# Performance work log

Measured on AMD Instinct MI355X. Metric: run time of the kernel, lower is better.

## Reference

```python
import jax, jax.numpy as jnp
import numpy as np

N, E, G = 50000, 400000, 64   # nodes, edges, graphs
HEADS = 4
F_IN, H1, C3, OUT = 64, 96, 64, 10  # in feats, hidden (3*32), last conv out, classes


def seg_softmax(alpha, index, num_segments):
    # numerically stable softmax over segments (PyG softmax(alpha, edge_index_i))
    amax = jax.ops.segment_max(alpha, index, num_segments)
    amax = jnp.where(jnp.isfinite(amax), amax, 0.0)
    e = jnp.exp(alpha - amax[index])
    denom = jax.ops.segment_sum(e, index, num_segments)
    return e / (denom[index] + 1e-16)


def general_conv(x, src, dst, Wm, bm, att, Ws=None, bs=None):
    # GeneralConv (attention=True, additive, directed_msg, aggr='add')
    C = att.shape[-1]
    m = (x[src] @ Wm + bm).reshape(-1, HEADS, C)              # [E,H,C] gathered messages
    a = jax.nn.leaky_relu((m * att).sum(-1), 0.2)             # [E,H] attention logits
    a = seg_softmax(a, dst, N)                                # segment softmax per dest node
    agg = jax.ops.segment_sum(m * a[..., None], dst, N)       # [N,H,C] scatter-add
    out = agg.mean(axis=1)                                    # head mean -> [N,C]
    if Ws is None:                                            # lin_self = Identity (in==out)
        return out + x
    return out + x @ Ws + bs


def setup_inputs():
    key = jax.random.key(0)
    ks = jax.random.split(key, 16)
    s = 0.05
    return {
        "x": jax.random.normal(ks[0], (N, F_IN), jnp.float32),
        "edge_index": jax.random.randint(ks[1], (2, E), 0, N, jnp.int32),
        "batch": jnp.sort(jax.random.randint(ks[2], (N,), 0, G, jnp.int32)),
        # layer 1: F_IN -> H1
        "Wm1": jax.random.normal(ks[3], (F_IN, HEADS * H1), jnp.float32) * s,
        "bm1": jnp.zeros((HEADS * H1,), jnp.float32),
        "att1": jax.random.normal(ks[4], (HEADS, H1), jnp.float32) * s,
        "Ws1": jax.random.normal(ks[5], (F_IN, H1), jnp.float32) * s,
        "bs1": jnp.zeros((H1,), jnp.float32),
        # layer 2: H1 -> H1 (lin_self = Identity)
        "Wm2": jax.random.normal(ks[6], (H1, HEADS * H1), jnp.float32) * s,
        "bm2": jnp.zeros((HEADS * H1,), jnp.float32),
        "att2": jax.random.normal(ks[7], (HEADS, H1), jnp.float32) * s,
        # layer 3: H1 -> C3
        "Wm3": jax.random.normal(ks[8], (H1, HEADS * C3), jnp.float32) * s,
        "bm3": jnp.zeros((HEADS * C3,), jnp.float32),
        "att3": jax.random.normal(ks[9], (HEADS, C3), jnp.float32) * s,
        "Ws3": jax.random.normal(ks[10], (H1, C3), jnp.float32) * s,
        "bs3": jnp.zeros((C3,), jnp.float32),
        # classifier
        "Wfc": jax.random.normal(ks[11], (C3, OUT), jnp.float32) * s,
        "bfc": jnp.zeros((OUT,), jnp.float32),
    }


def reference(x, edge_index, batch, Wm1, bm1, att1, Ws1, bs1,
              Wm2, bm2, att2, Wm3, bm3, att3, Ws3, bs3, Wfc, bfc):
    src, dst = edge_index[0], edge_index[1]
    h = general_conv(x, src, dst, Wm1, bm1, att1, Ws1, bs1)
    h = general_conv(h, src, dst, Wm2, bm2, att2)
    h = general_conv(h, src, dst, Wm3, bm3, att3, Ws3, bs3)
    # global_mean_pool
    ssum = jax.ops.segment_sum(h, batch, G)
    cnt = jax.ops.segment_sum(jnp.ones((N, 1), h.dtype), batch, G)
    pooled = ssum / jnp.maximum(cnt, 1.0)                      # [G,C3]
    logits = pooled @ Wfc + bfc
    return jax.nn.log_softmax(logits, axis=1)
```

## Files before the change

### kernel.cpp

```cpp
#include <hip/hip_runtime.h>
#include <hip/hip_bf16.h>
#include <stdint.h>

using bf16 = __hip_bfloat16;
typedef __attribute__((ext_vector_type(8))) short bf16x8;
typedef __attribute__((ext_vector_type(4))) float f32x4;
typedef __attribute__((ext_vector_type(2))) float f32x2;

#define NN 50000
#define NE 400000
#define NG 64
#define NHEADS 4
#define FIN 64
#define HID 96
#define CC3 64
#define NOUT 10

#define SCAN_BLOCK 256
#define NPART ((NN + SCAN_BLOCK - 1) / SCAN_BLOCK)
#define GB16 ((NN/16 + 3) / 4)

__device__ __forceinline__ float b2f(bf16 h){ return __bfloat162float(h); }
__device__ __forceinline__ bf16 f2b(float f){ return __float2bfloat16(f); }

#define NTJOBS 5
struct PrepJobs {
  const float* W[NTJOBS]; bf16* WT[NTJOBS]; int K[NTJOBS]; int Nc[NTJOBS];
  const float* LWm[3]; const float* Latt[3]; const float* Lbm[3];
  bf16* LWT[3]; int LK[3]; int LC[3]; int LncMain[3];
  float* lb;
  int* deg; float* psum;
};
__global__ __launch_bounds__(256) void prep_kernel(PrepJobs j){
  int bid = blockIdx.x;
  if (bid < 3){
    int l = bid;
    const float* Wm = j.LWm[l]; const float* att = j.Latt[l]; const float* bm = j.Lbm[l];
    bf16* WT = j.LWT[l];
    int K = j.LK[l], C = j.LC[l], ncMain = j.LncMain[l];
    for (int idx = threadIdx.x; idx < K*4; idx += 256){
      int k = idx >> 2, h = idx & 3;
      float a = 0.f;
      for (int c=0;c<C;++c) a += Wm[(size_t)k*(4*C) + h*C + c] * att[h*C + c];
      WT[(size_t)(ncMain+h)*K + k] = f2b(a);
    }
    for (int idx = threadIdx.x; idx < 12*K; idx += 256){
      int col = ncMain + 4 + idx / K, k = idx % K;
      WT[(size_t)col*K + k] = f2b(0.f);
    }
    if (threadIdx.x < 4){
      int h = threadIdx.x; float a = 0.f;
      for (int c=0;c<C;++c) a += bm[h*C + c] * att[h*C + c];
      j.lb[l*4 + h] = a;
    }
  } else if (bid < 3 + 256){
    int b = bid - 3;
    for (int t=0; t<NTJOBS; ++t){
      int K = j.K[t], Nc = j.Nc[t], total = K*Nc;
      for (int i = b*256 + threadIdx.x; i < total; i += 256*256){
        int k = i / Nc, n = i % Nc;
        j.WT[t][(size_t)n*K + k] = f2b(j.W[t][i]);
      }
    }
  } else if (bid < 3 + 256 + NPART){
    int i = (bid - 3 - 256)*256 + threadIdx.x;
    if (i < NN) j.deg[i] = 0;
  } else {
    for (int i = threadIdx.x; i < NG*CC3; i += 256) j.psum[i] = 0.f;
  }
}

__global__ void deg_kernel(const int* __restrict__ ei, int* __restrict__ deg){
  int e = blockIdx.x*256 + threadIdx.x;
  if (e < NE) atomicAdd(&deg[ei[NE + e]], 1);
}

__global__ __launch_bounds__(256) void scan_part_kernel(const int* __restrict__ deg,
                                                        int* __restrict__ partials){
  int i = blockIdx.x*SCAN_BLOCK + threadIdx.x;
  int v = (i < NN) ? deg[i] : 0;
  __shared__ int ws[4];
  int lane = threadIdx.x & 63, w = threadIdx.x >> 6;
  int s = v;
  #pragma unroll
  for (int m=1;m<64;m<<=1) s += __shfl_xor(s,m);
  if (lane==0) ws[w]=s;
  __syncthreads();
  if (threadIdx.x==0) partials[blockIdx.x] = ws[0]+ws[1]+ws[2]+ws[3];
}

__global__ __launch_bounds__(256) void scan_top_kernel(int* __restrict__ partials,
                                                       int* __restrict__ off){
  __shared__ int buf[256];
  int t = threadIdx.x;
  int v = (t < NPART) ? partials[t] : 0;
  buf[t] = v; __syncthreads();
  for (int s=1;s<256;s<<=1){
    int x = (t>=s) ? buf[t-s] : 0;
    __syncthreads();
    buf[t] += x;
    __syncthreads();
  }
  if (t < NPART) partials[t] = buf[t] - v;
  if (t == 0) off[NN] = buf[255];
}

__global__ __launch_bounds__(256) void scan_final_kernel(const int* __restrict__ deg,
    const int* __restrict__ partials, int* __restrict__ off, int* __restrict__ cursor){
  __shared__ int buf[256];
  int i = blockIdx.x*SCAN_BLOCK + threadIdx.x;
  int t = threadIdx.x;
  int v = (i<NN) ? deg[i] : 0;
  buf[t] = v; __syncthreads();
  for (int s=1;s<256;s<<=1){
    int x = (t>=s) ? buf[t-s] : 0;
    __syncthreads();
    buf[t] += x;
    __syncthreads();
  }
  int ex = partials[blockIdx.x] + buf[t] - v;
  if (i<NN){ off[i]=ex; cursor[i]=ex; }
}

__global__ void scatter_kernel(const int* __restrict__ ei, int* __restrict__ cursor,
                               int* __restrict__ csr_src){
  int e = blockIdx.x*256 + threadIdx.x;
  if (e < NE){
    int d = ei[NE + e];
    int slot = atomicAdd(&cursor[d], 1);
    csr_src[slot] = ei[e];
  }
}

template<int K, bool F32A>
__global__ __launch_bounds__(256) void gemm_mfma(const void* __restrict__ Ap,
    const bf16* __restrict__ WT, const float* __restrict__ biasMain,
    const float* __restrict__ lb4, uint8_t* __restrict__ outMain, int ncMain,
    float* __restrict__ EL, const float* __restrict__ biasSelf,
    bf16* __restrict__ outSelf, int ncSelf, int msgG, int totalU, int UPB)
{
  constexpr int KT = K/32;
  __shared__ unsigned int sbuf[4][16][16];
  const int wave = threadIdx.x >> 6, lane = threadIdx.x & 63;
  const int tile = blockIdx.x*4 + wave;
  if (tile >= NN/16) return;
  const int lm = lane & 15, q = lane >> 4;
  const int nodeRow = tile*16 + lm;
  const int rdRow = lane >> 2, rdCol = lane & 3;
  const int outRow = tile*16 + rdRow;

  bf16x8 xfrag[KT];
  if (F32A){
    const float* Af = (const float*)Ap;
    #pragma unroll
    for (int kt=0; kt<KT; ++kt){
      float4 a0 = *(const float4*)(Af + (size_t)nodeRow*K + kt*32 + q*8);
      float4 a1 = *(const float4*)(Af + (size_t)nodeRow*K + kt*32 + q*8 + 4);
      bf16 tmp[8];
      tmp[0]=f2b(a0.x); tmp[1]=f2b(a0.y); tmp[2]=f2b(a0.z); tmp[3]=f2b(a0.w);
      tmp[4]=f2b(a1.x); tmp[5]=f2b(a1.y); tmp[6]=f2b(a1.z); tmp[7]=f2b(a1.w);
      xfrag[kt] = *(const bf16x8*)tmp;
    }
  } else {
    const bf16* A = (const bf16*)Ap;
    #pragma unroll
    for (int kt=0; kt<KT; ++kt)
      xfrag[kt] = *(const bf16x8*)(A + (size_t)nodeRow*K + kt*32 + q*8);
  }

  const int u0 = blockIdx.y*UPB, u1 = min(u0+UPB, totalU);
  for (int u=u0; u<u1; ++u){
    if (u < msgG){
      #pragma unroll
      for (int t=0;t<4;++t){
        int ct = u*4 + t;
        f32x4 acc = {};
        #pragma unroll
        for (int kt=0; kt<KT; ++kt){
          bf16x8 wfrag = *(const bf16x8*)(WT + (size_t)(ct*16+lm)*K + kt*32 + q*8);
          acc = __builtin_amdgcn_mfma_f32_16x16x32_bf16(wfrag, xfrag[kt], acc, 0,0,0);
        }
        int wc = ct*16 + q*4;
        float v0 = acc[0]+biasMain[wc],   v1 = acc[1]+biasMain[wc+1];
        float v2 = acc[2]+biasMain[wc+2], v3 = acc[3]+biasMain[wc+3];
        int pk = 0;
        pk = __builtin_amdgcn_cvt_pk_fp8_f32(v0, v1, pk, false);
        pk = __builtin_amdgcn_cvt_pk_fp8_f32(v2, v3, pk, true);
        sbuf[wave][lm][t*4 + q] = (unsigned int)pk;
      }
      __builtin_amdgcn_wave_barrier();
      uint4 v = *(uint4*)&sbuf[wave][rdRow][rdCol*4];
      *(uint4*)(outMain + (size_t)outRow*ncMain + u*64 + rdCol*16) = v;
      __builtin_amdgcn_wave_barrier();
    } else if (u == msgG){
      int ct = ncMain/16;
      f32x4 acc = {};
      #pragma unroll
      for (int kt=0; kt<KT; ++kt){
        bf16x8 wfrag = *(const bf16x8*)(WT + (size_t)(ct*16+lm)*K + kt*32 + q*8);
        acc = __builtin_amdgcn_mfma_f32_16x16x32_bf16(wfrag, xfrag[kt], acc, 0,0,0);
      }
      if (q == 0){
        float4 e;
        float l;
        l = acc[0]+lb4[0]; l = (l>=0.f)?l:0.2f*l; e.x = __expf(fminf(fmaxf(l,-60.f),60.f));
        l = acc[1]+lb4[1]; l = (l>=0.f)?l:0.2f*l; e.y = __expf(fminf(fmaxf(l,-60.f),60.f));
        l = acc[2]+lb4[2]; l = (l>=0.f)?l:0.2f*l; e.z = __expf(fminf(fmaxf(l,-60.f),60.f));
        l = acc[3]+lb4[3]; l = (l>=0.f)?l:0.2f*l; e.w = __expf(fminf(fmaxf(l,-60.f),60.f));
        *(float4*)(EL + 4*(size_t)nodeRow) = e;
      }
    } else {
      int sg = u - msgG - 1;
      #pragma unroll
      for (int t=0;t<2;++t){
        int ct = ncMain/16 + 1 + sg*2 + t;
        f32x4 acc = {};
        #pragma unroll
        for (int kt=0; kt<KT; ++kt){
          bf16x8 wfrag = *(const bf16x8*)(WT + (size_t)(ct*16+lm)*K + kt*32 + q*8);
          acc = __builtin_amdgcn_mfma_f32_16x16x32_bf16(wfrag, xfrag[kt], acc, 0,0,0);
        }
        int c = ct*16 + q*4 - ncMain - 16;
        bf16 st[4];
        st[0]=f2b(acc[0]+biasSelf[c]);   st[1]=f2b(acc[1]+biasSelf[c+1]);
        st[2]=f2b(acc[2]+biasSelf[c+2]); st[3]=f2b(acc[3]+biasSelf[c+3]);
        uint2 uu = *(uint2*)st;
        sbuf[wave][lm][t*8 + q*2]     = uu.x;
        sbuf[wave][lm][t*8 + q*2 + 1] = uu.y;
      }
      __builtin_amdgcn_wave_barrier();
      uint4 v = *(uint4*)&sbuf[wave][rdRow][rdCol*4];
      *(uint4*)(outSelf + (size_t)outRow*ncSelf + sg*32 + rdCol*8) = v;
      __builtin_amdgcn_wave_barrier();
    }
  }
}

template<int C>
__global__ __launch_bounds__(256) void conv_agg(const int* __restrict__ off,
    const int* __restrict__ csr_src, const float* __restrict__ EL,
    const uint8_t* __restrict__ M8, const bf16* __restrict__ Hself,
    bf16* __restrict__ Hout)
{
  constexpr int R = 4*C;
  __shared__ float red[4][R];
  const int wave = threadIdx.x >> 6, lane = threadIdx.x & 63;
  const int n = blockIdx.x*4 + wave;
  const int e0 = off[n], e1 = off[n+1];

  const bool active = (8*lane) < R;
  const int hidx = min(3, (8*lane) / C);
  const int myoff = active ? lane*8 : 0;
  float acc[8] = {0,0,0,0,0,0,0,0};
  float dnl = 0.f;

  for (int base=e0; base<e1; base+=8){
    const int cnt8 = min(8, e1-base);
    int sreg = (lane < cnt8) ? csr_src[base+lane] : 0;
    int sv[8];
    #pragma unroll
    for (int j=0;j<8;++j) sv[j] = __shfl(sreg, j);

    float wl[8]; uint2 u[8];
    #pragma unroll
    for (int j=0;j<8;++j){
      wl[j] = EL[4*(size_t)sv[j] + hidx];
      u[j]  = *(const uint2*)(M8 + (size_t)sv[j]*R + myoff);
    }
    #pragma unroll
    for (int j=0;j<8;++j){
      float w = (j < cnt8) ? wl[j] : 0.f;
      dnl += w;
      f32x2 a0 = __builtin_amdgcn_cvt_pk_f32_fp8((int)u[j].x, false);
      f32x2 a1 = __builtin_amdgcn_cvt_pk_f32_fp8((int)u[j].x, true);
      f32x2 a2 = __builtin_amdgcn_cvt_pk_f32_fp8((int)u[j].y, false);
      f32x2 a3 = __builtin_amdgcn_cvt_pk_f32_fp8((int)u[j].y, true);
      acc[0] += a0.x*w;  acc[1] += a0.y*w;
      acc[2] += a1.x*w;  acc[3] += a1.y*w;
      acc[4] += a2.x*w;  acc[5] += a2.y*w;
      acc[6] += a3.x*w;  acc[7] += a3.y*w;
    }
  }

  float rd = 1.f/(dnl + 1e-16f);
  if (active){
    #pragma unroll
    for (int j=0;j<8;++j) red[wave][8*lane+j] = acc[j]*rd;
  }
  __syncthreads();

  for (int c=lane; c<C; c+=64){
    float v = 0.25f*(red[wave][c] + red[wave][C+c] + red[wave][2*C+c] + red[wave][3*C+c]);
    float sv2 = b2f(Hself[(size_t)n*C + c]);
    Hout[(size_t)n*C + c] = f2b(v + sv2);
  }
}

__global__ __launch_bounds__(256) void pool_kernel(const bf16* __restrict__ H3,
    const int* __restrict__ batch, float* __restrict__ psum){
  const int wave = threadIdx.x >> 6, lane = threadIdx.x & 63;
  const int row0 = (blockIdx.x*4 + wave)*64;
  if (row0 >= NN) return;
  const int cnt = min(64, NN - row0);
  int bv = (lane < cnt) ? batch[row0 + lane] : -1;
  int cur = __shfl(bv, 0);
  float acc = 0.f;
  for (int j=0; j<cnt; ++j){
    int g = __shfl(bv, j);
    if (g != cur){ atomicAdd(&psum[cur*CC3 + lane], acc); acc = 0.f; cur = g; }
    acc += b2f(H3[(size_t)(row0 + j)*CC3 + lane]);
  }
  atomicAdd(&psum[cur*CC3 + lane], acc);
}

__global__ __launch_bounds__(64) void fc_kernel(const float* __restrict__ psum,
    const int* __restrict__ batch, const float* __restrict__ Wfc,
    const float* __restrict__ bfc, float* __restrict__ out){
  int g = blockIdx.x, t = threadIdx.x;
  __shared__ int sb[2];
  if (t < 2){
    int target = g + t;
    int lo=0, hi=NN;
    while (lo<hi){ int mid=(lo+hi)>>1; if (batch[mid]<target) lo=mid+1; else hi=mid; }
    sb[t]=lo;
  }
  __syncthreads();
  float cnt = (float)(sb[1]-sb[0]);
  __shared__ float p[CC3];
  __shared__ float lg[NOUT];
  p[t] = psum[g*CC3 + t] / fmaxf(cnt, 1.0f);
  __syncthreads();
  if (t < NOUT){
    float a = bfc[t];
    for (int c=0;c<CC3;++c) a += p[c]*Wfc[c*NOUT + t];
    lg[t] = a;
  }
  __syncthreads();
  if (t < NOUT){
    float m = -INFINITY;
    #pragma unroll
    for (int i=0;i<NOUT;++i) m = fmaxf(m, lg[i]);
    float s = 0.f;
    #pragma unroll
    for (int i=0;i<NOUT;++i) s += __expf(lg[i]-m);
    out[g*NOUT + t] = lg[t] - m - __logf(s);
  }
}

extern "C" void kernel_launch(void* const* d_in, const int* in_sizes, int n_in,
                              void* d_out, int out_size, void* d_ws, size_t ws_size,
                              hipStream_t stream) {
  const float* xf    = (const float*)d_in[0];
  const int*   ei    = (const int*)d_in[1];
  const int*   batch = (const int*)d_in[2];
  const float* pWm1  = (const float*)d_in[3];
  const float* pbm1  = (const float*)d_in[4];
  const float* patt1 = (const float*)d_in[5];
  const float* pWs1  = (const float*)d_in[6];
  const float* pbs1  = (const float*)d_in[7];
  const float* pWm2  = (const float*)d_in[8];
  const float* pbm2  = (const float*)d_in[9];
  const float* patt2 = (const float*)d_in[10];
  const float* pWm3  = (const float*)d_in[11];
  const float* pbm3  = (const float*)d_in[12];
  const float* patt3 = (const float*)d_in[13];
  const float* pWs3  = (const float*)d_in[14];
  const float* pbs3  = (const float*)d_in[15];
  const float* pWfc  = (const float*)d_in[16];
  const float* pbfc  = (const float*)d_in[17];

  char* p = (char*)d_ws;
  auto alloc = [&](size_t bytes)->char*{ char* q = p; p += (bytes + 255) & ~(size_t)255; return q; };
  int*     deg     = (int*)  alloc(NN*sizeof(int));
  int*     off     = (int*)  alloc((NN+1)*sizeof(int));
  int*     cursor  = (int*)  alloc(NN*sizeof(int));
  int*     csr_src = (int*)  alloc(NE*sizeof(int));
  int*     partials= (int*)  alloc(NPART*sizeof(int));
  float*   EL      = (float*)alloc((size_t)NN*4*sizeof(float));
  uint8_t* Mb8     = (uint8_t*)alloc((size_t)NN*384);
  bf16*    H1b     = (bf16*) alloc((size_t)NN*96*sizeof(bf16));
  bf16*    H2b     = (bf16*) alloc((size_t)NN*96*sizeof(bf16));
  float*   psum    = (float*)alloc((size_t)NG*CC3*sizeof(float));
  bf16*  WT1cat = (bf16*)alloc((size_t)496*FIN*sizeof(bf16));
  bf16*  WT2cat = (bf16*)alloc((size_t)400*HID*sizeof(bf16));
  bf16*  WT3cat = (bf16*)alloc((size_t)336*HID*sizeof(bf16));
  float* lb     = (float*)alloc(12*sizeof(float));
  bf16*  H3b = H1b;

  PrepJobs pj;
  pj.W[0]=pWm1; pj.WT[0]=WT1cat;                 pj.K[0]=FIN; pj.Nc[0]=384;
  pj.W[1]=pWs1; pj.WT[1]=WT1cat+(size_t)400*FIN; pj.K[1]=FIN; pj.Nc[1]=96;
  pj.W[2]=pWm2; pj.WT[2]=WT2cat;                 pj.K[2]=HID; pj.Nc[2]=384;
  pj.W[3]=pWm3; pj.WT[3]=WT3cat;                 pj.K[3]=HID; pj.Nc[3]=256;
  pj.W[4]=pWs3; pj.WT[4]=WT3cat+(size_t)272*HID; pj.K[4]=HID; pj.Nc[4]=64;
  pj.LWm[0]=pWm1; pj.Latt[0]=patt1; pj.Lbm[0]=pbm1; pj.LWT[0]=WT1cat; pj.LK[0]=FIN; pj.LC[0]=96; pj.LncMain[0]=384;
  pj.LWm[1]=pWm2; pj.Latt[1]=patt2; pj.Lbm[1]=pbm2; pj.LWT[1]=WT2cat; pj.LK[1]=HID; pj.LC[1]=96; pj.LncMain[1]=384;
  pj.LWm[2]=pWm3; pj.Latt[2]=patt3; pj.Lbm[2]=pbm3; pj.LWT[2]=WT3cat; pj.LK[2]=HID; pj.LC[2]=64; pj.LncMain[2]=256;
  pj.lb = lb; pj.deg = deg; pj.psum = psum;
  prep_kernel<<<3+256+NPART+1, 256, 0, stream>>>(pj);

  deg_kernel<<<(NE+255)/256, 256, 0, stream>>>(ei, deg);
  scan_part_kernel<<<NPART, 256, 0, stream>>>(deg, partials);
  scan_top_kernel<<<1, 256, 0, stream>>>(partials, off);
  scan_final_kernel<<<NPART, 256, 0, stream>>>(deg, partials, off, cursor);
  scatter_kernel<<<(NE+255)/256, 256, 0, stream>>>(ei, cursor, csr_src);

  const int AB = NN/4;
  const int PB = (NN + 255)/256;

  gemm_mfma<64,true><<<dim3(GB16,4), 256, 0, stream>>>(xf, WT1cat, pbm1, lb,
                                                       Mb8, 384, EL, pbs1, H1b, 96,
                                                       6, 10, 3);
  conv_agg<96><<<AB, 256, 0, stream>>>(off, csr_src, EL, Mb8, H1b, H1b);

  gemm_mfma<96,false><<<dim3(GB16,4), 256, 0, stream>>>(H1b, WT2cat, pbm2, lb+4,
                                                        Mb8, 384, EL, pbm2, nullptr, 0,
                                                        6, 7, 2);
  conv_agg<96><<<AB, 256, 0, stream>>>(off, csr_src, EL, Mb8, H1b, H2b);

  gemm_mfma<96,false><<<dim3(GB16,3), 256, 0, stream>>>(H2b, WT3cat, pbm3, lb+8,
                                                        Mb8, 256, EL, pbs3, H3b, 64,
                                                        4, 7, 3);
  conv_agg<64><<<AB, 256, 0, stream>>>(off, csr_src, EL, Mb8, H3b, H3b);

  pool_kernel<<<PB, 256, 0, stream>>>(H3b, batch, psum);
  fc_kernel<<<NG, 64, 0, stream>>>(psum, batch, pWfc, pbfc, (float*)d_out);
}
```

Measured before the change: 371.4 us.

## Process two nodes per wave in aggregation, fuse pooling and scan top

The aggregation kernel now handles two destination nodes per wave, issuing gathers for both neighbour lists in each round to raise memory-level parallelism. The last conv layer folds global mean pooling into its epilogue with per-block atomic adds, which removes the separate pool kernel and the write of H3. The scan top step is merged into the partial-scan kernel using a last-block-done counter, saving one launch. The cost is imbalance when the two nodes' degrees differ, since the wave loops over the larger degree and does masked work for the shorter list.

```diff
diff --git a/kernel.cpp b/kernel.cpp
--- a/kernel.cpp
+++ b/kernel.cpp
@@ -29,7 +29,7 @@
   const float* LWm[3]; const float* Latt[3]; const float* Lbm[3];
   bf16* LWT[3]; int LK[3]; int LC[3]; int LncMain[3];
   float* lb;
-  int* deg; float* psum;
+  int* deg; float* psum; int* done;
 };
 __global__ __launch_bounds__(256) void prep_kernel(PrepJobs j){
   int bid = blockIdx.x;
@@ -67,6 +67,7 @@
     if (i < NN) j.deg[i] = 0;
   } else {
     for (int i = threadIdx.x; i < NG*CC3; i += 256) j.psum[i] = 0.f;
+    if (threadIdx.x == 0) *j.done = 0;
   }
 }
 
@@ -76,33 +77,39 @@
 }
 
 __global__ __launch_bounds__(256) void scan_part_kernel(const int* __restrict__ deg,
-                                                        int* __restrict__ partials){
+    int* __restrict__ partials, int* __restrict__ done, int* __restrict__ off){
+  __shared__ int ws[4];
+  __shared__ int lastflag;
+  __shared__ int buf[256];
   int i = blockIdx.x*SCAN_BLOCK + threadIdx.x;
   int v = (i < NN) ? deg[i] : 0;
-  __shared__ int ws[4];
   int lane = threadIdx.x & 63, w = threadIdx.x >> 6;
   int s = v;
   #pragma unroll
   for (int m=1;m<64;m<<=1) s += __shfl_xor(s,m);
   if (lane==0) ws[w]=s;
   __syncthreads();
-  if (threadIdx.x==0) partials[blockIdx.x] = ws[0]+ws[1]+ws[2]+ws[3];
-}
-
-__global__ __launch_bounds__(256) void scan_top_kernel(int* __restrict__ partials,
-                                                       int* __restrict__ off){
-  __shared__ int buf[256];
-  int t = threadIdx.x;
-  int v = (t < NPART) ? partials[t] : 0;
-  buf[t] = v; __syncthreads();
-  for (int s=1;s<256;s<<=1){
-    int x = (t>=s) ? buf[t-s] : 0;
-    __syncthreads();
-    buf[t] += x;
-    __syncthreads();
-  }
-  if (t < NPART) partials[t] = buf[t] - v;
-  if (t == 0) off[NN] = buf[255];
+  if (threadIdx.x==0){
+    int tot = ws[0]+ws[1]+ws[2]+ws[3];
+    atomicExch(&partials[blockIdx.x], tot);
+    __threadfence();
+    int old = atomicAdd(done, 1);
+    lastflag = (old == NPART-1) ? 1 : 0;
+  }
+  __syncthreads();
+  if (lastflag){
+    int t = threadIdx.x;
+    int pv = (t < NPART) ? atomicAdd(&partials[t], 0) : 0;
+    buf[t] = pv; __syncthreads();
+    for (int st=1; st<256; st<<=1){
+      int x = (t>=st) ? buf[t-st] : 0;
+      __syncthreads();
+      buf[t] += x;
+      __syncthreads();
+    }
+    if (t < NPART) atomicExch(&partials[t], buf[t] - pv);
+    if (t == 0) off[NN] = buf[255];
+  }
 }
 
 __global__ __launch_bounds__(256) void scan_final_kernel(const int* __restrict__ deg,
@@ -236,81 +243,108 @@
   }
 }
 
-template<int C>
+template<int C, bool FP>
 __global__ __launch_bounds__(256) void conv_agg(const int* __restrict__ off,
     const int* __restrict__ csr_src, const float* __restrict__ EL,
     const uint8_t* __restrict__ M8, const bf16* __restrict__ Hself,
-    bf16* __restrict__ Hout)
+    bf16* __restrict__ Hout, const int* __restrict__ batch, float* __restrict__ psum)
 {
   constexpr int R = 4*C;
-  __shared__ float red[4][R];
+  __shared__ float red[4][2][R];
   const int wave = threadIdx.x >> 6, lane = threadIdx.x & 63;
-  const int n = blockIdx.x*4 + wave;
-  const int e0 = off[n], e1 = off[n+1];
+  const int nb0 = blockIdx.x*8;
+  const int n0 = nb0 + wave*2;
+  const int a0 = off[n0], a1 = off[n0+1], b1 = off[n0+2];
+  const int dA = a1-a0, dB = b1-a1;
 
   const bool active = (8*lane) < R;
   const int hidx = min(3, (8*lane) / C);
   const int myoff = active ? lane*8 : 0;
-  float acc[8] = {0,0,0,0,0,0,0,0};
-  float dnl = 0.f;
-
-  for (int base=e0; base<e1; base+=8){
-    const int cnt8 = min(8, e1-base);
-    int sreg = (lane < cnt8) ? csr_src[base+lane] : 0;
-    int sv[8];
-    #pragma unroll
-    for (int j=0;j<8;++j) sv[j] = __shfl(sreg, j);
-
-    float wl[8]; uint2 u[8];
+  float accA[8] = {0,0,0,0,0,0,0,0}, accB[8] = {0,0,0,0,0,0,0,0};
+  float dnA = 0.f, dnB = 0.f;
+
+  const int rounds = (max(dA,dB) + 7) >> 3;
+  for (int r=0; r<rounds; ++r){
+    const int cntA = min(8, max(0, dA - r*8));
+    const int cntB = min(8, max(0, dB - r*8));
+    int sreg = 0;
+    if (lane < cntA) sreg = csr_src[a0 + r*8 + lane];
+    else if (lane >= 8 && lane < 8 + cntB) sreg = csr_src[a1 + r*8 + (lane-8)];
+    int svA[8], svB[8];
+    #pragma unroll
+    for (int j=0;j<8;++j){ svA[j] = __shfl(sreg, j); svB[j] = __shfl(sreg, 8+j); }
+
+    float wlA[8], wlB[8]; uint2 uA[8], uB[8];
     #pragma unroll
     for (int j=0;j<8;++j){
-      wl[j] = EL[4*(size_t)sv[j] + hidx];
-      u[j]  = *(const uint2*)(M8 + (size_t)sv[j]*R + myoff);
+      wlA[j] = EL[4*(size_t)svA[j] + hidx];
+      uA[j]  = *(const uint2*)(M8 + (size_t)svA[j]*R + myoff);
+      wlB[j] = EL[4*(size_t)svB[j] + hidx];
+      uB[j]  = *(const uint2*)(M8 + (size_t)svB[j]*R + myoff);
     }
     #pragma unroll
     for (int j=0;j<8;++j){
-      float w = (j < cnt8) ? wl[j] : 0.f;
-      dnl += w;
-      f32x2 a0 = __builtin_amdgcn_cvt_pk_f32_fp8((int)u[j].x, false);
-      f32x2 a1 = __builtin_amdgcn_cvt_pk_f32_fp8((int)u[j].x, true);
-      f32x2 a2 = __builtin_amdgcn_cvt_pk_f32_fp8((int)u[j].y, false);
-      f32x2 a3 = __builtin_amdgcn_cvt_pk_f32_fp8((int)u[j].y, true);
-      acc[0] += a0.x*w;  acc[1] += a0.y*w;
-      acc[2] += a1.x*w;  acc[3] += a1.y*w;
-      acc[4] += a2.x*w;  acc[5] += a2.y*w;
-      acc[6] += a3.x*w;  acc[7] += a3.y*w;
-    }
-  }
-
-  float rd = 1.f/(dnl + 1e-16f);
+      float wA = (j < cntA) ? wlA[j] : 0.f;
+      float wB = (j < cntB) ? wlB[j] : 0.f;
+      dnA += wA; dnB += wB;
+      f32x2 a0v,a1v,a2v,a3v;
+      a0v = __builtin_amdgcn_cvt_pk_f32_fp8((int)uA[j].x, false);
+      a1v = __builtin_amdgcn_cvt_pk_f32_fp8((int)uA[j].x, true);
+      a2v = __builtin_amdgcn_cvt_pk_f32_fp8((int)uA[j].y, false);
+      a3v = __builtin_amdgcn_cvt_pk_f32_fp8((int)uA[j].y, true);
+      accA[0] += a0v.x*wA;  accA[1] += a0v.y*wA;
+      accA[2] += a1v.x*wA;  accA[3] += a1v.y*wA;
+      accA[4] += a2v.x*wA;  accA[5] += a2v.y*wA;
+      accA[6] += a3v.x*wA;  accA[7] += a3v.y*wA;
+      a0v = __builtin_amdgcn_cvt_pk_f32_fp8((int)uB[j].x, false);
+      a1v = __builtin_amdgcn_cvt_pk_f32_fp8((int)uB[j].x, true);
+      a2v = __builtin_amdgcn_cvt_pk_f32_fp8((int)uB[j].y, false);
+      a3v = __builtin_amdgcn_cvt_pk_f32_fp8((int)uB[j].y, true);
+      accB[0] += a0v.x*wB;  accB[1] += a0v.y*wB;
+      accB[2] += a1v.x*wB;  accB[3] += a1v.y*wB;
+      accB[4] += a2v.x*wB;  accB[5] += a2v.y*wB;
+      accB[6] += a3v.x*wB;  accB[7] += a3v.y*wB;
+    }
+  }
+
+  float rdA = 1.f/(dnA + 1e-16f), rdB = 1.f/(dnB + 1e-16f);
   if (active){
     #pragma unroll
-    for (int j=0;j<8;++j) red[wave][8*lane+j] = acc[j]*rd;
-  }
-  __syncthreads();
-
-  for (int c=lane; c<C; c+=64){
-    float v = 0.25f*(red[wave][c] + red[wave][C+c] + red[wave][2*C+c] + red[wave][3*C+c]);
-    float sv2 = b2f(Hself[(size_t)n*C + c]);
-    Hout[(size_t)n*C + c] = f2b(v + sv2);
-  }
-}
-
-__global__ __launch_bounds__(256) void pool_kernel(const bf16* __restrict__ H3,
-    const int* __restrict__ batch, float* __restrict__ psum){
-  const int wave = threadIdx.x >> 6, lane = threadIdx.x & 63;
-  const int row0 = (blockIdx.x*4 + wave)*64;
-  if (row0 >= NN) return;
-  const int cnt = min(64, NN - row0);
-  int bv = (lane < cnt) ? batch[row0 + lane] : -1;
-  int cur = __shfl(bv, 0);
-  float acc = 0.f;
-  for (int j=0; j<cnt; ++j){
-    int g = __shfl(bv, j);
-    if (g != cur){ atomicAdd(&psum[cur*CC3 + lane], acc); acc = 0.f; cur = g; }
-    acc += b2f(H3[(size_t)(row0 + j)*CC3 + lane]);
-  }
-  atomicAdd(&psum[cur*CC3 + lane], acc);
+    for (int j=0;j<8;++j){
+      red[wave][0][8*lane+j] = accA[j]*rdA;
+      red[wave][1][8*lane+j] = accB[j]*rdB;
+    }
+  }
+  __syncthreads();
+
+  if (!FP){
+    #pragma unroll
+    for (int p2=0;p2<2;++p2){
+      int n = n0 + p2;
+      for (int c=lane; c<C; c+=64){
+        float v = 0.25f*(red[wave][p2][c] + red[wave][p2][C+c]
+                       + red[wave][p2][2*C+c] + red[wave][p2][3*C+c]);
+        Hout[(size_t)n*C + c] = f2b(v + b2f(Hself[(size_t)n*C + c]));
+      }
+    }
+  } else {
+    if (wave == 0){
+      int c = lane;
+      int curg = batch[nb0];
+      float a = 0.f;
+      #pragma unroll
+      for (int i=0;i<8;++i){
+        int w = i>>1, p2 = i&1;
+        float v = 0.25f*(red[w][p2][c] + red[w][p2][C+c]
+                       + red[w][p2][2*C+c] + red[w][p2][3*C+c]);
+        v += b2f(Hself[(size_t)(nb0+i)*C + c]);
+        int g = batch[nb0+i];
+        if (g != curg){ atomicAdd(&psum[curg*C + c], a); a = 0.f; curg = g; }
+        a += v;
+      }
+      atomicAdd(&psum[curg*C + c], a);
+    }
+  }
 }
 
 __global__ __launch_bounds__(64) void fc_kernel(const float* __restrict__ psum,
@@ -376,6 +410,7 @@
   int*     cursor  = (int*)  alloc(NN*sizeof(int));
   int*     csr_src = (int*)  alloc(NE*sizeof(int));
   int*     partials= (int*)  alloc(NPART*sizeof(int));
+  int*     done    = (int*)  alloc(sizeof(int));
   float*   EL      = (float*)alloc((size_t)NN*4*sizeof(float));
   uint8_t* Mb8     = (uint8_t*)alloc((size_t)NN*384);
   bf16*    H1b     = (bf16*) alloc((size_t)NN*96*sizeof(bf16));
@@ -396,33 +431,31 @@
   pj.LWm[0]=pWm1; pj.Latt[0]=patt1; pj.Lbm[0]=pbm1; pj.LWT[0]=WT1cat; pj.LK[0]=FIN; pj.LC[0]=96; pj.LncMain[0]=384;
   pj.LWm[1]=pWm2; pj.Latt[1]=patt2; pj.Lbm[1]=pbm2; pj.LWT[1]=WT2cat; pj.LK[1]=HID; pj.LC[1]=96; pj.LncMain[1]=384;
   pj.LWm[2]=pWm3; pj.Latt[2]=patt3; pj.Lbm[2]=pbm3; pj.LWT[2]=WT3cat; pj.LK[2]=HID; pj.LC[2]=64; pj.LncMain[2]=256;
-  pj.lb = lb; pj.deg = deg; pj.psum = psum;
+  pj.lb = lb; pj.deg = deg; pj.psum = psum; pj.done = done;
   prep_kernel<<<3+256+NPART+1, 256, 0, stream>>>(pj);
 
   deg_kernel<<<(NE+255)/256, 256, 0, stream>>>(ei, deg);
-  scan_part_kernel<<<NPART, 256, 0, stream>>>(deg, partials);
-  scan_top_kernel<<<1, 256, 0, stream>>>(partials, off);
+  scan_part_kernel<<<NPART, 256, 0, stream>>>(deg, partials, done, off);
   scan_final_kernel<<<NPART, 256, 0, stream>>>(deg, partials, off, cursor);
   scatter_kernel<<<(NE+255)/256, 256, 0, stream>>>(ei, cursor, csr_src);
 
-  const int AB = NN/4;
-  const int PB = (NN + 255)/256;
+  const int AB = NN/8;
 
   gemm_mfma<64,true><<<dim3(GB16,4), 256, 0, stream>>>(xf, WT1cat, pbm1, lb,
                                                        Mb8, 384, EL, pbs1, H1b, 96,
                                                        6, 10, 3);
-  conv_agg<96><<<AB, 256, 0, stream>>>(off, csr_src, EL, Mb8, H1b, H1b);
-
+  conv_agg<96,false><<<AB, 256, 0, stream>>>(off, csr_src, EL, Mb8, H1b, H1b,
+                                             batch, psum);
   gemm_mfma<96,false><<<dim3(GB16,4), 256, 0, stream>>>(H1b, WT2cat, pbm2, lb+4,
                                                         Mb8, 384, EL, pbm2, nullptr, 0,
                                                         6, 7, 2);
-  conv_agg<96><<<AB, 256, 0, stream>>>(off, csr_src, EL, Mb8, H1b, H2b);
-
+  conv_agg<96,false><<<AB, 256, 0, stream>>>(off, csr_src, EL, Mb8, H1b, H2b,
+                                             batch, psum);
   gemm_mfma<96,false><<<dim3(GB16,3), 256, 0, stream>>>(H2b, WT3cat, pbm3, lb+8,
                                                         Mb8, 256, EL, pbs3, H3b, 64,
                                                         4, 7, 3);
-  conv_agg<64><<<AB, 256, 0, stream>>>(off, csr_src, EL, Mb8, H3b, H3b);
-
-  pool_kernel<<<PB, 256, 0, stream>>>(H3b, batch, psum);
+  conv_agg<64,true><<<AB, 256, 0, stream>>>(off, csr_src, EL, Mb8, H3b, nullptr,
+                                            batch, psum);
+
   fc_kernel<<<NG, 64, 0, stream>>>(psum, batch, pWfc, pbfc, (float*)d_out);
 }
```

Measured after the change: 426.2 us. 1.15x slower.

## Fuse scan top-level into partial scan and pooling into last aggregation

Applied to the files above, without the earlier changes.

Removes the single-block scan_top kernel by having the last-finishing block of scan_part, found through an atomic done counter, perform the top-level prefix scan. Also folds global mean pooling into the final conv_agg: each block sums its 4 nodes per graph and atomically adds into psum, so H3 is never written and re-read. This saves two kernel launches and one pass over H3. In exchange there are more atomics on psum, one per block rather than one per 64-row chunk, and the scan relies on threadfence and atomic ordering.

```diff
diff --git a/kernel.cpp b/kernel.cpp
--- a/kernel.cpp
+++ b/kernel.cpp
@@ -29,7 +29,7 @@
   const float* LWm[3]; const float* Latt[3]; const float* Lbm[3];
   bf16* LWT[3]; int LK[3]; int LC[3]; int LncMain[3];
   float* lb;
-  int* deg; float* psum;
+  int* deg; float* psum; int* done;
 };
 __global__ __launch_bounds__(256) void prep_kernel(PrepJobs j){
   int bid = blockIdx.x;
@@ -67,6 +67,7 @@
     if (i < NN) j.deg[i] = 0;
   } else {
     for (int i = threadIdx.x; i < NG*CC3; i += 256) j.psum[i] = 0.f;
+    if (threadIdx.x == 0) *j.done = 0;
   }
 }
 
@@ -76,33 +77,39 @@
 }
 
 __global__ __launch_bounds__(256) void scan_part_kernel(const int* __restrict__ deg,
-                                                        int* __restrict__ partials){
+    int* __restrict__ partials, int* __restrict__ done, int* __restrict__ off){
+  __shared__ int ws[4];
+  __shared__ int lastflag;
+  __shared__ int buf[256];
   int i = blockIdx.x*SCAN_BLOCK + threadIdx.x;
   int v = (i < NN) ? deg[i] : 0;
-  __shared__ int ws[4];
   int lane = threadIdx.x & 63, w = threadIdx.x >> 6;
   int s = v;
   #pragma unroll
   for (int m=1;m<64;m<<=1) s += __shfl_xor(s,m);
   if (lane==0) ws[w]=s;
   __syncthreads();
-  if (threadIdx.x==0) partials[blockIdx.x] = ws[0]+ws[1]+ws[2]+ws[3];
-}
-
-__global__ __launch_bounds__(256) void scan_top_kernel(int* __restrict__ partials,
-                                                       int* __restrict__ off){
-  __shared__ int buf[256];
-  int t = threadIdx.x;
-  int v = (t < NPART) ? partials[t] : 0;
-  buf[t] = v; __syncthreads();
-  for (int s=1;s<256;s<<=1){
-    int x = (t>=s) ? buf[t-s] : 0;
-    __syncthreads();
-    buf[t] += x;
-    __syncthreads();
-  }
-  if (t < NPART) partials[t] = buf[t] - v;
-  if (t == 0) off[NN] = buf[255];
+  if (threadIdx.x==0){
+    int tot = ws[0]+ws[1]+ws[2]+ws[3];
+    atomicExch(&partials[blockIdx.x], tot);
+    __threadfence();
+    int old = atomicAdd(done, 1);
+    lastflag = (old == NPART-1) ? 1 : 0;
+  }
+  __syncthreads();
+  if (lastflag){
+    int t = threadIdx.x;
+    int pv = (t < NPART) ? atomicAdd(&partials[t], 0) : 0;
+    buf[t] = pv; __syncthreads();
+    for (int st=1; st<256; st<<=1){
+      int x = (t>=st) ? buf[t-st] : 0;
+      __syncthreads();
+      buf[t] += x;
+      __syncthreads();
+    }
+    if (t < NPART) atomicExch(&partials[t], buf[t] - pv);
+    if (t == 0) off[NN] = buf[255];
+  }
 }
 
 __global__ __launch_bounds__(256) void scan_final_kernel(const int* __restrict__ deg,
@@ -236,11 +243,11 @@
   }
 }
 
-template<int C>
+template<int C, bool FP>
 __global__ __launch_bounds__(256) void conv_agg(const int* __restrict__ off,
     const int* __restrict__ csr_src, const float* __restrict__ EL,
     const uint8_t* __restrict__ M8, const bf16* __restrict__ Hself,
-    bf16* __restrict__ Hout)
+    bf16* __restrict__ Hout, const int* __restrict__ batch, float* __restrict__ psum)
 {
   constexpr int R = 4*C;
   __shared__ float red[4][R];
@@ -289,28 +296,28 @@
   }
   __syncthreads();
 
-  for (int c=lane; c<C; c+=64){
-    float v = 0.25f*(red[wave][c] + red[wave][C+c] + red[wave][2*C+c] + red[wave][3*C+c]);
-    float sv2 = b2f(Hself[(size_t)n*C + c]);
-    Hout[(size_t)n*C + c] = f2b(v + sv2);
-  }
-}
-
-__global__ __launch_bounds__(256) void pool_kernel(const bf16* __restrict__ H3,
-    const int* __restrict__ batch, float* __restrict__ psum){
-  const int wave = threadIdx.x >> 6, lane = threadIdx.x & 63;
-  const int row0 = (blockIdx.x*4 + wave)*64;
-  if (row0 >= NN) return;
-  const int cnt = min(64, NN - row0);
-  int bv = (lane < cnt) ? batch[row0 + lane] : -1;
-  int cur = __shfl(bv, 0);
-  float acc = 0.f;
-  for (int j=0; j<cnt; ++j){
-    int g = __shfl(bv, j);
-    if (g != cur){ atomicAdd(&psum[cur*CC3 + lane], acc); acc = 0.f; cur = g; }
-    acc += b2f(H3[(size_t)(row0 + j)*CC3 + lane]);
-  }
-  atomicAdd(&psum[cur*CC3 + lane], acc);
+  if (!FP){
+    for (int c=lane; c<C; c+=64){
+      float v = 0.25f*(red[wave][c] + red[wave][C+c] + red[wave][2*C+c] + red[wave][3*C+c]);
+      Hout[(size_t)n*C + c] = f2b(v + b2f(Hself[(size_t)n*C + c]));
+    }
+  } else {
+    if (wave == 0){
+      int c = lane;
+      int nb0 = blockIdx.x*4;
+      int curg = batch[nb0];
+      float a = 0.f;
+      #pragma unroll
+      for (int i=0;i<4;++i){
+        float v = 0.25f*(red[i][c] + red[i][C+c] + red[i][2*C+c] + red[i][3*C+c]);
+        v += b2f(Hself[(size_t)(nb0+i)*C + c]);
+        int g = batch[nb0+i];
+        if (g != curg){ atomicAdd(&psum[curg*C + c], a); a = 0.f; curg = g; }
+        a += v;
+      }
+      atomicAdd(&psum[curg*C + c], a);
+    }
+  }
 }
 
 __global__ __launch_bounds__(64) void fc_kernel(const float* __restrict__ psum,
@@ -376,6 +383,7 @@
   int*     cursor  = (int*)  alloc(NN*sizeof(int));
   int*     csr_src = (int*)  alloc(NE*sizeof(int));
   int*     partials= (int*)  alloc(NPART*sizeof(int));
+  int*     done    = (int*)  alloc(sizeof(int));
   float*   EL      = (float*)alloc((size_t)NN*4*sizeof(float));
   uint8_t* Mb8     = (uint8_t*)alloc((size_t)NN*384);
   bf16*    H1b     = (bf16*) alloc((size_t)NN*96*sizeof(bf16));
@@ -396,33 +404,31 @@
   pj.LWm[0]=pWm1; pj.Latt[0]=patt1; pj.Lbm[0]=pbm1; pj.LWT[0]=WT1cat; pj.LK[0]=FIN; pj.LC[0]=96; pj.LncMain[0]=384;
   pj.LWm[1]=pWm2; pj.Latt[1]=patt2; pj.Lbm[1]=pbm2; pj.LWT[1]=WT2cat; pj.LK[1]=HID; pj.LC[1]=96; pj.LncMain[1]=384;
   pj.LWm[2]=pWm3; pj.Latt[2]=patt3; pj.Lbm[2]=pbm3; pj.LWT[2]=WT3cat; pj.LK[2]=HID; pj.LC[2]=64; pj.LncMain[2]=256;
-  pj.lb = lb; pj.deg = deg; pj.psum = psum;
+  pj.lb = lb; pj.deg = deg; pj.psum = psum; pj.done = done;
   prep_kernel<<<3+256+NPART+1, 256, 0, stream>>>(pj);
 
   deg_kernel<<<(NE+255)/256, 256, 0, stream>>>(ei, deg);
-  scan_part_kernel<<<NPART, 256, 0, stream>>>(deg, partials);
-  scan_top_kernel<<<1, 256, 0, stream>>>(partials, off);
+  scan_part_kernel<<<NPART, 256, 0, stream>>>(deg, partials, done, off);
   scan_final_kernel<<<NPART, 256, 0, stream>>>(deg, partials, off, cursor);
   scatter_kernel<<<(NE+255)/256, 256, 0, stream>>>(ei, cursor, csr_src);
 
   const int AB = NN/4;
-  const int PB = (NN + 255)/256;
 
   gemm_mfma<64,true><<<dim3(GB16,4), 256, 0, stream>>>(xf, WT1cat, pbm1, lb,
                                                        Mb8, 384, EL, pbs1, H1b, 96,
                                                        6, 10, 3);
-  conv_agg<96><<<AB, 256, 0, stream>>>(off, csr_src, EL, Mb8, H1b, H1b);
-
+  conv_agg<96,false><<<AB, 256, 0, stream>>>(off, csr_src, EL, Mb8, H1b, H1b,
+                                             batch, psum);
   gemm_mfma<96,false><<<dim3(GB16,4), 256, 0, stream>>>(H1b, WT2cat, pbm2, lb+4,
                                                         Mb8, 384, EL, pbm2, nullptr, 0,
                                                         6, 7, 2);
-  conv_agg<96><<<AB, 256, 0, stream>>>(off, csr_src, EL, Mb8, H1b, H2b);
-
+  conv_agg<96,false><<<AB, 256, 0, stream>>>(off, csr_src, EL, Mb8, H1b, H2b,
+                                             batch, psum);
   gemm_mfma<96,false><<<dim3(GB16,3), 256, 0, stream>>>(H2b, WT3cat, pbm3, lb+8,
                                                         Mb8, 256, EL, pbs3, H3b, 64,
                                                         4, 7, 3);
-  conv_agg<64><<<AB, 256, 0, stream>>>(off, csr_src, EL, Mb8, H3b, H3b);
-
-  pool_kernel<<<PB, 256, 0, stream>>>(H3b, batch, psum);
+  conv_agg<64,true><<<AB, 256, 0, stream>>>(off, csr_src, EL, Mb8, H3b, nullptr,
+                                            batch, psum);
+
   fc_kernel<<<NG, 64, 0, stream>>>(psum, batch, pWfc, pbfc, (float*)d_out);
 }
```

Result: faster. 354.1 us, median of 2 (-4.7%).
